# Kernel tuning notes

Measured on AMD Instinct MI355X. Metric: run time of the kernel, lower is better.

The kernel has to match this reference:

```python
import jax, jax.numpy as jnp
import numpy as np

B, Q, C, H, NSTEPS = 1024, 96, 16, 100, 100  # batch, q (MA order), channels, hidden, Euler steps


def setup_inputs() -> dict:
    key = jax.random.key(0)
    ks = jax.random.split(key, 6)
    s = 0.1  # weight init scale
    return {
        "series": jax.random.normal(ks[0], (B, Q, C), jnp.float32),
        "rand_error": jax.random.normal(ks[1], (B, 1, C), jnp.float32),
        "W1": jax.random.normal(ks[2], (H, Q + 2), jnp.float32) * s,
        "b1": jnp.zeros((H,), jnp.float32),
        "W2": jax.random.normal(ks[3], (H, H), jnp.float32) * s,
        "b2": jnp.zeros((H,), jnp.float32),
        "W3": jax.random.normal(ks[4], (Q + 1, H), jnp.float32) * s,
        "b3": jnp.zeros((Q + 1,), jnp.float32),
    }


def _mlp(x, t, W1, b1, W2, b2, W3, b3):
    # x: (B, Q+1, C), t: (B, 1, C)  -> cat along feature dim, permute to (B, C, Q+2)
    inp = jnp.concatenate([x, t], axis=1).transpose(0, 2, 1)
    h = jnp.tanh(inp @ W1.T + b1)
    h = jnp.tanh(h @ W2.T + b2)
    out = h @ W3.T + b3            # (B, C, Q+1)
    return out.transpose(0, 2, 1)  # (B, Q+1, C)


def reference(series, rand_error, W1, b1, W2, b2, W3, b3):
    # ma_forecast sampling path: noise = cat(series, rand_error) then Euler flow sampling
    noise = jnp.concatenate([series, rand_error], axis=1)  # (B, Q+1, C)
    dt = jnp.float32(1.0 / NSTEPS)

    def step(x, i):
        t = jnp.ones((x.shape[0], 1, x.shape[2]), x.dtype) * (i.astype(x.dtype) / NSTEPS)
        pred = _mlp(x, t, W1, b1, W2, b2, W3, b3)
        return x + (pred - noise) * dt, None

    x, _ = jax.lax.scan(step, noise, jnp.arange(NSTEPS))
    return x
```

## Files before the change

kernel.cpp:

```cpp
#include <hip/hip_runtime.h>


#define NB 1024
#define NQ 96
#define NC 16
#define NH 100
#define QP1 97
#define QP2 98
#define ROWS 16
#define NTHR 256
#define STR 136
#define NSTEPS_ 100

typedef __attribute__((ext_vector_type(8))) short bf16x8;
typedef __attribute__((ext_vector_type(4))) float f32x4;
typedef __attribute__((ext_vector_type(2))) unsigned uintx2;

__device__ __forceinline__ short f2bf_rne(float f) {
  unsigned u = __builtin_bit_cast(unsigned, f);
  u = u + 0x7fffu + ((u >> 16) & 1u);
  return (short)(u >> 16);
}

__device__ __forceinline__ unsigned bfhi(float f) {
  return (__builtin_bit_cast(unsigned, f) + 0x8000u) >> 16;
}

__device__ __forceinline__ unsigned pack_bf2(float a, float b) {
  unsigned ua = __builtin_bit_cast(unsigned, a) + 0x8000u;
  unsigned ub = __builtin_bit_cast(unsigned, b) + 0x8000u;
  return __builtin_amdgcn_perm(ub, ua, 0x07060302);
}

__device__ __forceinline__ float fast_tanh(float x) {
  float e = __builtin_amdgcn_exp2f(x * 2.88539008177792681f);
  float r = __builtin_amdgcn_rcpf(e + 1.0f);
  return fmaf(-2.0f, r, 1.0f);
}

__device__ void load_afrag(const float* __restrict__ W,
                           const float* __restrict__ bias, int ws, int mvalid,
                           int KW, int m, int quad, bf16x8 dst[4]) {
#pragma unroll
  for (int kb = 0; kb < 4; ++kb) {
    bf16x8 v;
#pragma unroll
    for (int i = 0; i < 8; ++i) {
      int k = kb * 32 + quad * 8 + i;
      float f = 0.0f;
      if (m < mvalid) {
        if (k < KW) f = W[m * ws + k];
        else if (k == KW) f = bias[m];
      }
      v[i] = f2bf_rne(f);
    }
    dst[kb] = v;
  }
}

__device__ __forceinline__ void gemm2(const short* __restrict__ src, int rbase,
                                      const bf16x8 (&A)[2][4], f32x4 (&acc)[2]) {
  acc[0] = {0.0f, 0.0f, 0.0f, 0.0f};
  acc[1] = {0.0f, 0.0f, 0.0f, 0.0f};
#pragma unroll
  for (int kb = 0; kb < 4; ++kb) {
    bf16x8 bv = *(const bf16x8*)(src + rbase + kb * 32);
    acc[0] = __builtin_amdgcn_mfma_f32_16x16x32_bf16(A[0][kb], bv, acc[0], 0, 0, 0);
    acc[1] = __builtin_amdgcn_mfma_f32_16x16x32_bf16(A[1][kb], bv, acc[1], 0, 0, 0);
  }
}

__device__ __forceinline__ void store_h(short* __restrict__ dst, int wb0,
                                        int wb1, bool fix100, f32x4 (&acc)[2]) {
#pragma unroll
  for (int mtl = 0; mtl < 2; ++mtl) {
    unsigned u0 = pack_bf2(fast_tanh(acc[mtl][0]), fast_tanh(acc[mtl][1]));
    unsigned u1 = pack_bf2(fast_tanh(acc[mtl][2]), fast_tanh(acc[mtl][3]));
    if (mtl == 0 && fix100) u0 = (u0 & 0xFFFF0000u) | 0x3F80u;
    uintx2 v;
    v.x = u0;
    v.y = u1;
    *(uintx2*)(dst + (mtl ? wb1 : wb0)) = v;
  }
}

__device__ __forceinline__ void write_x(short* __restrict__ dst, int wb0,
                                        int wb1, bool fix96, unsigned tbits,
                                        f32x4 (&xm)[2]) {
#pragma unroll
  for (int mtl = 0; mtl < 2; ++mtl) {
    unsigned u0 = pack_bf2(xm[mtl][0], xm[mtl][1]);
    unsigned u1 = pack_bf2(xm[mtl][2], xm[mtl][3]);
    if (mtl == 0 && fix96) {
      u0 = (u0 & 0x0000FFFFu) | (tbits << 16);
      u1 = 0x00003F80u;
    }
    uintx2 v;
    v.x = u0;
    v.y = u1;
    *(uintx2*)(dst + (mtl ? wb1 : wb0)) = v;
  }
}

__global__ void __launch_bounds__(NTHR, 3)
arima_mfma_t(const float* __restrict__ series,
             const float* __restrict__ rand_error,
             const float* __restrict__ W1, const float* __restrict__ b1,
             const float* __restrict__ W2, const float* __restrict__ b2,
             const float* __restrict__ W3, const float* __restrict__ b3,
             float* __restrict__ out) {
  __shared__ __align__(16) short bufP[ROWS * STR];
  __shared__ __align__(16) short bufQ[ROWS * STR];

  const int tid = threadIdx.x;
  const int w = tid >> 6, l = tid & 63;
  const int col = l & 15, quad = l >> 4;
  const int mt0 = 2 * w;
  const int bglob = (int)blockIdx.x;

  bf16x8 afr[3][2][4];
#pragma unroll
  for (int mtl = 0; mtl < 2; ++mtl) {
    int m = (mt0 + mtl) * 16 + col;
    load_afrag(W1, b1, QP2, NH, QP2, m, quad, afr[0][mtl]);
    load_afrag(W2, b2, NH, NH, NH, m, quad, afr[1][mtl]);
    load_afrag(W3, b3, NH, QP1, NH, m, quad, afr[2][mtl]);
  }

  f32x4 xm[2], ns[2];
#pragma unroll
  for (int mtl = 0; mtl < 2; ++mtl)
#pragma unroll
    for (int r = 0; r < 4; ++r) {
      int q = (mt0 + mtl) * 16 + quad * 4 + r;
      float f = 0.0f;
      if (q < NQ) f = series[(bglob * NQ + q) * NC + col];
      else if (q == NQ) f = rand_error[bglob * NC + col];
      xm[mtl][r] = f;
      ns[mtl][r] = f;
    }

  const int wb0 = col * STR + (mt0 + 0) * 16 + quad * 4;
  const int wb1 = col * STR + (mt0 + 1) * 16 + quad * 4;
  const int base0 = (mt0 + 0) * 16 + quad * 4;
  const bool fix100 = (base0 == 100);
  const bool fix96 = (base0 == 96);
  const int rbase = col * STR + quad * 8;

  write_x(bufP, wb0, wb1, fix96, 0u , xm);
  __syncthreads();

  short* bx = bufP;
  short* bh = bufQ;

#pragma unroll 1
  for (int step = 0; step < NSTEPS_; ++step) {
    f32x4 acc[2];
    gemm2(bx, rbase, afr[0], acc);
    store_h(bh, wb0, wb1, fix100, acc);
    __syncthreads();
    gemm2(bh, rbase, afr[1], acc);
    store_h(bx, wb0, wb1, fix100, acc);
    __syncthreads();
    gemm2(bx, rbase, afr[2], acc);
#pragma unroll
    for (int mtl = 0; mtl < 2; ++mtl)
#pragma unroll
      for (int r = 0; r < 4; ++r)
        xm[mtl][r] = fmaf(acc[mtl][r] - ns[mtl][r], 0.01f, xm[mtl][r]);
    float t1 = (float)(step + 1) / 100.0f;
    write_x(bh, wb0, wb1, fix96, bfhi(t1), xm);
    __syncthreads();

    short* tp = bx;
    bx = bh;
    bh = tp;
  }

#pragma unroll
  for (int mtl = 0; mtl < 2; ++mtl)
#pragma unroll
    for (int r = 0; r < 4; ++r) {
      int q = (mt0 + mtl) * 16 + quad * 4 + r;
      if (q < QP1) out[(bglob * QP1 + q) * NC + col] = xm[mtl][r];
    }
}

extern "C" void kernel_launch(void* const* d_in, const int* in_sizes, int n_in,
                              void* d_out, int out_size, void* d_ws,
                              size_t ws_size, hipStream_t stream) {
  const float* series = (const float*)d_in[0];
  const float* rand_error = (const float*)d_in[1];
  const float* W1 = (const float*)d_in[2];
  const float* b1 = (const float*)d_in[3];
  const float* W2 = (const float*)d_in[4];
  const float* b2 = (const float*)d_in[5];
  const float* W3 = (const float*)d_in[6];
  const float* b3 = (const float*)d_in[7];
  float* out = (float*)d_out;

  dim3 grid(NB);
  dim3 block(NTHR);
  hipLaunchKernelGGL(arima_mfma_t, grid, block, 0, stream, series, rand_error,
                     W1, b1, W2, b2, W3, b3, out);
}
```

Measured before the change: 290.1 us.

## Process two batch rows per block with split weight tiles and rational tanh

```diff
diff --git a/kernel.cpp b/kernel.cpp
--- a/kernel.cpp
+++ b/kernel.cpp
@@ -7,7 +7,7 @@
 #define NH 100
 #define QP1 97
 #define QP2 98
-#define ROWS 16
+#define ROWS 32
 #define NTHR 256
 #define STR 136
 #define NSTEPS_ 100
@@ -33,9 +33,11 @@
 }
 
 __device__ __forceinline__ float fast_tanh(float x) {
-  float e = __builtin_amdgcn_exp2f(x * 2.88539008177792681f);
-  float r = __builtin_amdgcn_rcpf(e + 1.0f);
-  return fmaf(-2.0f, r, 1.0f);
+  float u = x * x;
+  float num = x * fmaf(u + 105.0f, u, 945.0f);
+  float den = fmaf(fmaf(15.0f, u, 420.0f), u, 945.0f);
+  float v = num * __builtin_amdgcn_rcpf(den);
+  return fminf(fmaxf(v, -1.0f), 1.0f);
 }
 
 __device__ void load_afrag(const float* __restrict__ W,
@@ -58,132 +60,200 @@
   }
 }
 
-__device__ __forceinline__ void gemm2(const short* __restrict__ src, int rbase,
-                                      const bf16x8 (&A)[2][4], f32x4 (&acc)[2]) {
-  acc[0] = {0.0f, 0.0f, 0.0f, 0.0f};
-  acc[1] = {0.0f, 0.0f, 0.0f, 0.0f};
+template <int TC>
+__device__ __forceinline__ void gemmN(const short* __restrict__ src, int rbase,
+                                      const bf16x8 (&A)[TC][4],
+                                      f32x4 (&acc)[TC]) {
+#pragma unroll
+  for (int t = 0; t < TC; ++t) acc[t] = {0.0f, 0.0f, 0.0f, 0.0f};
 #pragma unroll
   for (int kb = 0; kb < 4; ++kb) {
     bf16x8 bv = *(const bf16x8*)(src + rbase + kb * 32);
-    acc[0] = __builtin_amdgcn_mfma_f32_16x16x32_bf16(A[0][kb], bv, acc[0], 0, 0, 0);
-    acc[1] = __builtin_amdgcn_mfma_f32_16x16x32_bf16(A[1][kb], bv, acc[1], 0, 0, 0);
-  }
-}
-
-__device__ __forceinline__ void store_h(short* __restrict__ dst, int wb0,
-                                        int wb1, bool fix100, f32x4 (&acc)[2]) {
-#pragma unroll
-  for (int mtl = 0; mtl < 2; ++mtl) {
-    unsigned u0 = pack_bf2(fast_tanh(acc[mtl][0]), fast_tanh(acc[mtl][1]));
-    unsigned u1 = pack_bf2(fast_tanh(acc[mtl][2]), fast_tanh(acc[mtl][3]));
-    if (mtl == 0 && fix100) u0 = (u0 & 0xFFFF0000u) | 0x3F80u;
-    uintx2 v;
-    v.x = u0;
-    v.y = u1;
-    *(uintx2*)(dst + (mtl ? wb1 : wb0)) = v;
-  }
-}
-
-__device__ __forceinline__ void write_x(short* __restrict__ dst, int wb0,
-                                        int wb1, bool fix96, unsigned tbits,
-                                        f32x4 (&xm)[2]) {
-#pragma unroll
-  for (int mtl = 0; mtl < 2; ++mtl) {
-    unsigned u0 = pack_bf2(xm[mtl][0], xm[mtl][1]);
-    unsigned u1 = pack_bf2(xm[mtl][2], xm[mtl][3]);
-    if (mtl == 0 && fix96) {
-      u0 = (u0 & 0x0000FFFFu) | (tbits << 16);
-      u1 = 0x00003F80u;
-    }
-    uintx2 v;
-    v.x = u0;
-    v.y = u1;
-    *(uintx2*)(dst + (mtl ? wb1 : wb0)) = v;
-  }
-}
-
-__global__ void __launch_bounds__(NTHR, 3)
-arima_mfma_t(const float* __restrict__ series,
-             const float* __restrict__ rand_error,
-             const float* __restrict__ W1, const float* __restrict__ b1,
-             const float* __restrict__ W2, const float* __restrict__ b2,
-             const float* __restrict__ W3, const float* __restrict__ b3,
-             float* __restrict__ out) {
+#pragma unroll
+    for (int t = 0; t < TC; ++t)
+      acc[t] = __builtin_amdgcn_mfma_f32_16x16x32_bf16(A[t][kb], bv, acc[t], 0, 0, 0);
+  }
+}
+
+template <int TC, int TO>
+__device__ __forceinline__ void store_h(short* __restrict__ dst, int wrow,
+                                        int quad, f32x4 (&acc)[TC]) {
+#pragma unroll
+  for (int t = 0; t < TC; ++t) {
+    unsigned u0 = pack_bf2(fast_tanh(acc[t][0]), fast_tanh(acc[t][1]));
+    unsigned u1 = pack_bf2(fast_tanh(acc[t][2]), fast_tanh(acc[t][3]));
+    if constexpr (TO + 0 <= 6 && 6 < TO + TC) {
+      if (TO + t == 6 && quad == 1) u0 = (u0 & 0xFFFF0000u) | 0x3F80u;
+    }
+    uintx2 v; v.x = u0; v.y = u1;
+    *(uintx2*)(dst + wrow + (TO + t) * 16 + quad * 4) = v;
+  }
+}
+
+template <int TC, int TO>
+__device__ __forceinline__ void write_x(short* __restrict__ dst, int wrow,
+                                        int quad, unsigned tbits,
+                                        f32x4 (&xm)[TC]) {
+#pragma unroll
+  for (int t = 0; t < TC; ++t) {
+    unsigned u0 = pack_bf2(xm[t][0], xm[t][1]);
+    unsigned u1 = pack_bf2(xm[t][2], xm[t][3]);
+    if constexpr (TO + 0 <= 6 && 6 < TO + TC) {
+      if (TO + t == 6 && quad == 0) {
+        u0 = (u0 & 0x0000FFFFu) | (tbits << 16);
+        u1 = 0x00003F80u;
+      }
+    }
+    uintx2 v; v.x = u0; v.y = u1;
+    *(uintx2*)(dst + wrow + (TO + t) * 16 + quad * 4) = v;
+  }
+}
+
+template <int TC1, int TO1, int TC2, int TO2, int TC3, int TO3>
+__device__ __forceinline__ void run_all(
+    const float* __restrict__ series, const float* __restrict__ rand_error,
+    const float* __restrict__ W1, const float* __restrict__ b1,
+    const float* __restrict__ W2, const float* __restrict__ b2,
+    const float* __restrict__ W3, const float* __restrict__ b3,
+    float* __restrict__ out, short* bufP, short* bufQ, int rw, int col,
+    int quad, int blk) {
+  bf16x8 a1[TC1][4], a2[TC2][4], a3[TC3][4];
+#pragma unroll
+  for (int t = 0; t < TC1; ++t)
+    load_afrag(W1, b1, QP2, NH, QP2, (TO1 + t) * 16 + col, quad, a1[t]);
+#pragma unroll
+  for (int t = 0; t < TC2; ++t)
+    load_afrag(W2, b2, NH, NH, NH, (TO2 + t) * 16 + col, quad, a2[t]);
+#pragma unroll
+  for (int t = 0; t < TC3; ++t)
+    load_afrag(W3, b3, NH, QP1, NH, (TO3 + t) * 16 + col, quad, a3[t]);
+
+  const int grow = blk * ROWS + rw * 16 + col;
+  const int gb = grow >> 4, gc = grow & 15;
+
+  f32x4 x0[TC3], xm[TC3];
+#pragma unroll
+  for (int t = 0; t < TC3; ++t)
+#pragma unroll
+    for (int r = 0; r < 4; ++r) {
+      int q = (TO3 + t) * 16 + quad * 4 + r;
+      float f = 0.0f;
+      if (q < NQ) f = series[(gb * NQ + q) * NC + gc];
+      else if (q == NQ) f = rand_error[gb * NC + gc];
+      x0[t][r] = f;
+      xm[t][r] = f;
+    }
+
+  const int wrow = (rw * 16 + col) * STR;
+  const int rbase = wrow + quad * 8;
+
+  write_x<TC3, TO3>(bufP, wrow, quad, 0u , xm);
+  __syncthreads();
+
+  short* bx = bufP;
+  short* bh = bufQ;
+
+#pragma unroll 1
+  for (int step = 0; step < NSTEPS_; ++step) {
+    {
+      f32x4 acc[TC1];
+      gemmN<TC1>(bx, rbase, a1, acc);
+      store_h<TC1, TO1>(bh, wrow, quad, acc);
+    }
+    __syncthreads();
+    {
+      f32x4 acc[TC2];
+      gemmN<TC2>(bh, rbase, a2, acc);
+      store_h<TC2, TO2>(bx, wrow, quad, acc);
+    }
+    __syncthreads();
+    {
+      f32x4 acc[TC3];
+      gemmN<TC3>(bx, rbase, a3, acc);
+#pragma unroll
+      for (int t = 0; t < TC3; ++t)
+#pragma unroll
+        for (int r = 0; r < 4; ++r)
+          xm[t][r] = fmaf(acc[t][r] - x0[t][r], 0.01f, xm[t][r]);
+      float t1 = (float)(step + 1) * 0.01f;
+      write_x<TC3, TO3>(bh, wrow, quad, bfhi(t1), xm);
+    }
+    __syncthreads();
+    short* tp = bx; bx = bh; bh = tp;
+  }
+
+#pragma unroll
+  for (int t = 0; t < TC3; ++t)
+#pragma unroll
+    for (int r = 0; r < 4; ++r) {
+      int q = (TO3 + t) * 16 + quad * 4 + r;
+      if (q < QP1) out[(gb * QP1 + q) * NC + gc] = xm[t][r];
+    }
+}
+
+__global__ void __launch_bounds__(NTHR, 2)
+arima_r4(const float* __restrict__ series, const float* __restrict__ rand_error,
+         const float* __restrict__ W1, const float* __restrict__ b1,
+         const float* __restrict__ W2, const float* __restrict__ b2,
+         const float* __restrict__ W3, const float* __restrict__ b3,
+         float* __restrict__ out) {
   __shared__ __align__(16) short bufP[ROWS * STR];
   __shared__ __align__(16) short bufQ[ROWS * STR];
 
   const int tid = threadIdx.x;
   const int w = tid >> 6, l = tid & 63;
   const int col = l & 15, quad = l >> 4;
-  const int mt0 = 2 * w;
-  const int bglob = (int)blockIdx.x;
-
-  bf16x8 afr[3][2][4];
-#pragma unroll
-  for (int mtl = 0; mtl < 2; ++mtl) {
-    int m = (mt0 + mtl) * 16 + col;
-    load_afrag(W1, b1, QP2, NH, QP2, m, quad, afr[0][mtl]);
-    load_afrag(W2, b2, NH, NH, NH, m, quad, afr[1][mtl]);
-    load_afrag(W3, b3, NH, QP1, NH, m, quad, afr[2][mtl]);
-  }
-
-  f32x4 xm[2], ns[2];
-#pragma unroll
-  for (int mtl = 0; mtl < 2; ++mtl)
-#pragma unroll
-    for (int r = 0; r < 4; ++r) {
-      int q = (mt0 + mtl) * 16 + quad * 4 + r;
-      float f = 0.0f;
-      if (q < NQ) f = series[(bglob * NQ + q) * NC + col];
-      else if (q == NQ) f = rand_error[bglob * NC + col];
-      xm[mtl][r] = f;
-      ns[mtl][r] = f;
-    }
-
-  const int wb0 = col * STR + (mt0 + 0) * 16 + quad * 4;
-  const int wb1 = col * STR + (mt0 + 1) * 16 + quad * 4;
-  const int base0 = (mt0 + 0) * 16 + quad * 4;
-  const bool fix100 = (base0 == 100);
-  const bool fix96 = (base0 == 96);
-  const int rbase = col * STR + quad * 8;
-
-  write_x(bufP, wb0, wb1, fix96, 0u , xm);
+  const int rw = w >> 1, nw = w & 1;
+
+  {
+    int* zp = (int*)bufP;
+    int* zq = (int*)bufQ;
+    for (int i = tid; i < ROWS * STR / 2; i += NTHR) { zp[i] = 0; zq[i] = 0; }
+  }
   __syncthreads();
 
-  short* bx = bufP;
-  short* bh = bufQ;
-
-#pragma unroll 1
-  for (int step = 0; step < NSTEPS_; ++step) {
-    f32x4 acc[2];
-    gemm2(bx, rbase, afr[0], acc);
-    store_h(bh, wb0, wb1, fix100, acc);
-    __syncthreads();
-    gemm2(bh, rbase, afr[1], acc);
-    store_h(bx, wb0, wb1, fix100, acc);
-    __syncthreads();
-    gemm2(bx, rbase, afr[2], acc);
-#pragma unroll
-    for (int mtl = 0; mtl < 2; ++mtl)
-#pragma unroll
-      for (int r = 0; r < 4; ++r)
-        xm[mtl][r] = fmaf(acc[mtl][r] - ns[mtl][r], 0.01f, xm[mtl][r]);
-    float t1 = (float)(step + 1) / 100.0f;
-    write_x(bh, wb0, wb1, fix96, bfhi(t1), xm);
-    __syncthreads();
-
-    short* tp = bx;
-    bx = bh;
-    bh = tp;
-  }
-
-#pragma unroll
-  for (int mtl = 0; mtl < 2; ++mtl)
-#pragma unroll
-    for (int r = 0; r < 4; ++r) {
-      int q = (mt0 + mtl) * 16 + quad * 4 + r;
-      if (q < QP1) out[(bglob * QP1 + q) * NC + col] = xm[mtl][r];
-    }
+  if (nw == 0) {
+    run_all<4, 0, 3, 0, 4, 0>(series, rand_error, W1, b1, W2, b2, W3, b3,
+                              (float*)nullptr ? nullptr : nullptr, bufP, bufQ,
+                              rw, col, quad, (int)blockIdx.x),
+        (void)0;
+  }
+  if (nw == 0) {
+  }
+  if (nw == 0) {
+  }
+}
+
+
+__global__ void __launch_bounds__(NTHR, 2)
+arima_r4_real(const float* __restrict__ series,
+              const float* __restrict__ rand_error,
+              const float* __restrict__ W1, const float* __restrict__ b1,
+              const float* __restrict__ W2, const float* __restrict__ b2,
+              const float* __restrict__ W3, const float* __restrict__ b3,
+              float* __restrict__ out) {
+  __shared__ __align__(16) short bufP[ROWS * STR];
+  __shared__ __align__(16) short bufQ[ROWS * STR];
+
+  const int tid = threadIdx.x;
+  const int w = tid >> 6, l = tid & 63;
+  const int col = l & 15, quad = l >> 4;
+  const int rw = w >> 1, nw = w & 1;
+
+  {
+    int* zp = (int*)bufP;
+    int* zq = (int*)bufQ;
+    for (int i = tid; i < ROWS * STR / 2; i += NTHR) { zp[i] = 0; zq[i] = 0; }
+  }
+  __syncthreads();
+
+  if (nw == 0) {
+    run_all<4, 0, 3, 0, 4, 0>(series, rand_error, W1, b1, W2, b2, W3, b3, out,
+                              bufP, bufQ, rw, col, quad, (int)blockIdx.x);
+  } else {
+    run_all<3, 4, 4, 3, 3, 4>(series, rand_error, W1, b1, W2, b2, W3, b3, out,
+                              bufP, bufQ, rw, col, quad, (int)blockIdx.x);
+  }
 }
 
 extern "C" void kernel_launch(void* const* d_in, const int* in_sizes, int n_in,
@@ -199,8 +269,8 @@
   const float* b3 = (const float*)d_in[7];
   float* out = (float*)d_out;
 
-  dim3 grid(NB);
+  dim3 grid((NB * NC) / ROWS);
   dim3 block(NTHR);
-  hipLaunchKernelGGL(arima_mfma_t, grid, block, 0, stream, series, rand_error,
+  hipLaunchKernelGGL(arima_r4_real, grid, block, 0, stream, series, rand_error,
                      W1, b1, W2, b2, W3, b3, out);
 }
```

Result: slower. 321.3 us (+10.7%).

## Fold W1·W3 into a precomputed matrix and update layer-1 pre-activations directly

Applied to the files above, without the earlier changes.

```diff
diff --git a/kernel.cpp b/kernel.cpp
--- a/kernel.cpp
+++ b/kernel.cpp
@@ -7,10 +7,10 @@
 #define NH 100
 #define QP1 97
 #define QP2 98
-#define ROWS 16
 #define NTHR 256
 #define STR 136
 #define NSTEPS_ 100
+#define MT_K 128
 
 typedef __attribute__((ext_vector_type(8))) short bf16x8;
 typedef __attribute__((ext_vector_type(4))) float f32x4;
@@ -22,10 +22,6 @@
   return (short)(u >> 16);
 }
 
-__device__ __forceinline__ unsigned bfhi(float f) {
-  return (__builtin_bit_cast(unsigned, f) + 0x8000u) >> 16;
-}
-
 __device__ __forceinline__ unsigned pack_bf2(float a, float b) {
   unsigned ua = __builtin_bit_cast(unsigned, a) + 0x8000u;
   unsigned ub = __builtin_bit_cast(unsigned, b) + 0x8000u;
@@ -33,9 +29,36 @@
 }
 
 __device__ __forceinline__ float fast_tanh(float x) {
-  float e = __builtin_amdgcn_exp2f(x * 2.88539008177792681f);
-  float r = __builtin_amdgcn_rcpf(e + 1.0f);
-  return fmaf(-2.0f, r, 1.0f);
+  float u = x * x;
+  float num = x * fmaf(u + 105.0f, u, 945.0f);
+  float den = fmaf(fmaf(15.0f, u, 420.0f), u, 945.0f);
+  float v = num * __builtin_amdgcn_rcpf(den);
+  return fminf(fmaxf(v, -1.0f), 1.0f);
+}
+
+__global__ void __launch_bounds__(128) arima_prep(
+    const float* __restrict__ W1, const float* __restrict__ b1,
+    const float* __restrict__ W3, const float* __restrict__ b3,
+    short* __restrict__ Mt, float* __restrict__ sv) {
+  const int n = blockIdx.x;
+  const int k = threadIdx.x;
+  float acc = 0.0f;
+  if (n < NH && k < NH) {
+#pragma unroll 1
+    for (int j = 0; j < QP1; ++j)
+      acc = fmaf(W1[n * QP2 + j], W3[j * NH + k], acc);
+  }
+  Mt[n * MT_K + k] = f2bf_rne(0.01f * acc);
+  if (k == 0) {
+    float s = 0.0f;
+    if (n < NH) {
+      float d = 0.0f;
+#pragma unroll 1
+      for (int j = 0; j < QP1; ++j) d = fmaf(W1[n * QP2 + j], b3[j], d);
+      s = 0.01f * (d + b1[n] + W1[n * QP2 + QP1]);
+    }
+    sv[n] = s;
+  }
 }
 
 __device__ void load_afrag(const float* __restrict__ W,
@@ -58,10 +81,9 @@
   }
 }
 
-__device__ __forceinline__ void gemm2(const short* __restrict__ src, int rbase,
-                                      const bf16x8 (&A)[2][4], f32x4 (&acc)[2]) {
-  acc[0] = {0.0f, 0.0f, 0.0f, 0.0f};
-  acc[1] = {0.0f, 0.0f, 0.0f, 0.0f};
+__device__ __forceinline__ void gemm_acc(const short* __restrict__ src,
+                                         int rbase, const bf16x8 (&A)[2][4],
+                                         f32x4 (&acc)[2]) {
 #pragma unroll
   for (int kb = 0; kb < 4; ++kb) {
     bf16x8 bv = *(const bf16x8*)(src + rbase + kb * 32);
@@ -70,120 +92,146 @@
   }
 }
 
-__device__ __forceinline__ void store_h(short* __restrict__ dst, int wb0,
-                                        int wb1, bool fix100, f32x4 (&acc)[2]) {
-#pragma unroll
-  for (int mtl = 0; mtl < 2; ++mtl) {
-    unsigned u0 = pack_bf2(fast_tanh(acc[mtl][0]), fast_tanh(acc[mtl][1]));
-    unsigned u1 = pack_bf2(fast_tanh(acc[mtl][2]), fast_tanh(acc[mtl][3]));
-    if (mtl == 0 && fix100) u0 = (u0 & 0xFFFF0000u) | 0x3F80u;
-    uintx2 v;
-    v.x = u0;
-    v.y = u1;
-    *(uintx2*)(dst + (mtl ? wb1 : wb0)) = v;
-  }
-}
-
-__device__ __forceinline__ void write_x(short* __restrict__ dst, int wb0,
-                                        int wb1, bool fix96, unsigned tbits,
-                                        f32x4 (&xm)[2]) {
-#pragma unroll
-  for (int mtl = 0; mtl < 2; ++mtl) {
-    unsigned u0 = pack_bf2(xm[mtl][0], xm[mtl][1]);
-    unsigned u1 = pack_bf2(xm[mtl][2], xm[mtl][3]);
-    if (mtl == 0 && fix96) {
-      u0 = (u0 & 0x0000FFFFu) | (tbits << 16);
-      u1 = 0x00003F80u;
-    }
-    uintx2 v;
-    v.x = u0;
-    v.y = u1;
-    *(uintx2*)(dst + (mtl ? wb1 : wb0)) = v;
-  }
+__device__ __forceinline__ void write_tiles(short* __restrict__ dst, int wrow,
+                                            int T0, int quad, const f32x4& v0,
+                                            const f32x4& v1) {
+  uintx2 a, b;
+  a.x = pack_bf2(v0[0], v0[1]);
+  a.y = pack_bf2(v0[2], v0[3]);
+  b.x = pack_bf2(v1[0], v1[1]);
+  b.y = pack_bf2(v1[2], v1[3]);
+  *(uintx2*)(dst + wrow + T0 * 16 + quad * 4) = a;
+  *(uintx2*)(dst + wrow + (T0 + 1) * 16 + quad * 4) = b;
 }
 
 __global__ void __launch_bounds__(NTHR, 3)
-arima_mfma_t(const float* __restrict__ series,
-             const float* __restrict__ rand_error,
-             const float* __restrict__ W1, const float* __restrict__ b1,
-             const float* __restrict__ W2, const float* __restrict__ b2,
-             const float* __restrict__ W3, const float* __restrict__ b3,
-             float* __restrict__ out) {
-  __shared__ __align__(16) short bufP[ROWS * STR];
-  __shared__ __align__(16) short bufQ[ROWS * STR];
+arima_r5(const float* __restrict__ series, const float* __restrict__ rand_error,
+         const float* __restrict__ W1, const float* __restrict__ b1,
+         const float* __restrict__ W2, const float* __restrict__ b2,
+         const float* __restrict__ W3, const float* __restrict__ b3,
+         const short* __restrict__ Mt, const float* __restrict__ sv,
+         float* __restrict__ out) {
+  __shared__ __align__(16) short buf1[16 * STR];
+  __shared__ __align__(16) short buf2[16 * STR];
 
   const int tid = threadIdx.x;
   const int w = tid >> 6, l = tid & 63;
   const int col = l & 15, quad = l >> 4;
-  const int mt0 = 2 * w;
-  const int bglob = (int)blockIdx.x;
-
-  bf16x8 afr[3][2][4];
-#pragma unroll
-  for (int mtl = 0; mtl < 2; ++mtl) {
-    int m = (mt0 + mtl) * 16 + col;
-    load_afrag(W1, b1, QP2, NH, QP2, m, quad, afr[0][mtl]);
-    load_afrag(W2, b2, NH, NH, NH, m, quad, afr[1][mtl]);
-    load_afrag(W3, b3, NH, QP1, NH, m, quad, afr[2][mtl]);
-  }
-
-  f32x4 xm[2], ns[2];
-#pragma unroll
-  for (int mtl = 0; mtl < 2; ++mtl)
-#pragma unroll
-    for (int r = 0; r < 4; ++r) {
-      int q = (mt0 + mtl) * 16 + quad * 4 + r;
-      float f = 0.0f;
-      if (q < NQ) f = series[(bglob * NQ + q) * NC + col];
-      else if (q == NQ) f = rand_error[bglob * NC + col];
-      xm[mtl][r] = f;
-      ns[mtl][r] = f;
-    }
-
-  const int wb0 = col * STR + (mt0 + 0) * 16 + quad * 4;
-  const int wb1 = col * STR + (mt0 + 1) * 16 + quad * 4;
-  const int base0 = (mt0 + 0) * 16 + quad * 4;
-  const bool fix100 = (base0 == 100);
-  const bool fix96 = (base0 == 96);
-  const int rbase = col * STR + quad * 8;
-
-  write_x(bufP, wb0, wb1, fix96, 0u , xm);
+  const int b = blockIdx.x;
+  const int T0 = 2 * w;
+  const int wrow = col * STR;
+  const int rbase = wrow + quad * 8;
+  const bool fixw = (w == 3 && quad == 1);
+
+  {
+    f32x4 xv[2];
+#pragma unroll
+    for (int t = 0; t < 2; ++t)
+#pragma unroll
+      for (int r = 0; r < 4; ++r) {
+        int q = (T0 + t) * 16 + quad * 4 + r;
+        float f = 0.0f;
+        if (q < NQ) f = series[(b * NQ + q) * NC + col];
+        else if (q == NQ) f = rand_error[b * NC + col];
+        else if (q == QP2) f = 1.0f;
+        xv[t][r] = f;
+      }
+    write_tiles(buf2, wrow, T0, quad, xv[0], xv[1]);
+  }
   __syncthreads();
 
-  short* bx = bufP;
-  short* bh = bufQ;
+  f32x4 z[2], v[2];
+  {
+    bf16x8 a1[2][4];
+#pragma unroll
+    for (int t = 0; t < 2; ++t)
+      load_afrag(W1, b1, QP2, NH, QP2, (T0 + t) * 16 + col, quad, a1[t]);
+    z[0] = {0.0f, 0.0f, 0.0f, 0.0f};
+    z[1] = {0.0f, 0.0f, 0.0f, 0.0f};
+    gemm_acc(buf2, rbase, a1, z);
+#pragma unroll
+    for (int t = 0; t < 2; ++t)
+#pragma unroll
+      for (int r = 0; r < 4; ++r)
+        v[t][r] = sv[(T0 + t) * 16 + quad * 4 + r] - 0.01f * z[t][r];
+  }
+  {
+    f32x4 h[2];
+#pragma unroll
+    for (int t = 0; t < 2; ++t)
+#pragma unroll
+      for (int r = 0; r < 4; ++r) h[t][r] = fast_tanh(z[t][r]);
+    if (fixw) h[0][0] = 1.0f;
+    write_tiles(buf1, wrow, T0, quad, h[0], h[1]);
+  }
+  __syncthreads();
+
+  bf16x8 a2[2][4], am[2][4];
+#pragma unroll
+  for (int t = 0; t < 2; ++t) {
+    load_afrag(W2, b2, NH, NH, NH, (T0 + t) * 16 + col, quad, a2[t]);
+#pragma unroll
+    for (int kb = 0; kb < 4; ++kb)
+      am[t][kb] = *(const bf16x8*)(Mt + ((T0 + t) * 16 + col) * MT_K +
+                                   kb * 32 + quad * 8);
+  }
+  f32x4 h2s[2] = {{0.0f, 0.0f, 0.0f, 0.0f}, {0.0f, 0.0f, 0.0f, 0.0f}};
 
 #pragma unroll 1
   for (int step = 0; step < NSTEPS_; ++step) {
-    f32x4 acc[2];
-    gemm2(bx, rbase, afr[0], acc);
-    store_h(bh, wb0, wb1, fix100, acc);
+    f32x4 acc[2], h[2];
+    acc[0] = {0.0f, 0.0f, 0.0f, 0.0f};
+    acc[1] = {0.0f, 0.0f, 0.0f, 0.0f};
+    gemm_acc(buf1, rbase, a2, acc);
+#pragma unroll
+    for (int t = 0; t < 2; ++t)
+#pragma unroll
+      for (int r = 0; r < 4; ++r) {
+        h[t][r] = fast_tanh(acc[t][r]);
+        h2s[t][r] += h[t][r];
+      }
+    write_tiles(buf2, wrow, T0, quad, h[0], h[1]);
     __syncthreads();
-    gemm2(bh, rbase, afr[1], acc);
-    store_h(bx, wb0, wb1, fix100, acc);
+    gemm_acc(buf2, rbase, am, z);
+#pragma unroll
+    for (int t = 0; t < 2; ++t)
+#pragma unroll
+      for (int r = 0; r < 4; ++r) {
+        z[t][r] += v[t][r];
+        h[t][r] = fast_tanh(z[t][r]);
+      }
+    if (fixw) h[0][0] = 1.0f;
+    write_tiles(buf1, wrow, T0, quad, h[0], h[1]);
     __syncthreads();
-    gemm2(bx, rbase, afr[2], acc);
-#pragma unroll
-    for (int mtl = 0; mtl < 2; ++mtl)
-#pragma unroll
-      for (int r = 0; r < 4; ++r)
-        xm[mtl][r] = fmaf(acc[mtl][r] - ns[mtl][r], 0.01f, xm[mtl][r]);
-    float t1 = (float)(step + 1) / 100.0f;
-    write_x(bh, wb0, wb1, fix96, bfhi(t1), xm);
-    __syncthreads();
-
-    short* tp = bx;
-    bx = bh;
-    bh = tp;
-  }
-
-#pragma unroll
-  for (int mtl = 0; mtl < 2; ++mtl)
-#pragma unroll
-    for (int r = 0; r < 4; ++r) {
-      int q = (mt0 + mtl) * 16 + quad * 4 + r;
-      if (q < QP1) out[(bglob * QP1 + q) * NC + col] = xm[mtl][r];
-    }
+  }
+
+  {
+    f32x4 ha[2];
+#pragma unroll
+    for (int t = 0; t < 2; ++t)
+#pragma unroll
+      for (int r = 0; r < 4; ++r) ha[t][r] = 0.01f * h2s[t][r];
+    if (fixw) ha[0][0] = 1.0f;
+    write_tiles(buf2, wrow, T0, quad, ha[0], ha[1]);
+  }
+  __syncthreads();
+  {
+    bf16x8 a3[2][4];
+#pragma unroll
+    for (int t = 0; t < 2; ++t)
+      load_afrag(W3, b3, NH, QP1, NH, (T0 + t) * 16 + col, quad, a3[t]);
+    f32x4 o[2];
+    o[0] = {0.0f, 0.0f, 0.0f, 0.0f};
+    o[1] = {0.0f, 0.0f, 0.0f, 0.0f};
+    gemm_acc(buf2, rbase, a3, o);
+#pragma unroll
+    for (int t = 0; t < 2; ++t)
+#pragma unroll
+      for (int r = 0; r < 4; ++r) {
+        int q = (T0 + t) * 16 + quad * 4 + r;
+        if (q < QP1) out[(b * QP1 + q) * NC + col] = o[t][r];
+      }
+  }
 }
 
 extern "C" void kernel_launch(void* const* d_in, const int* in_sizes, int n_in,
@@ -199,8 +247,11 @@
   const float* b3 = (const float*)d_in[7];
   float* out = (float*)d_out;
 
-  dim3 grid(NB);
-  dim3 block(NTHR);
-  hipLaunchKernelGGL(arima_mfma_t, grid, block, 0, stream, series, rand_error,
-                     W1, b1, W2, b2, W3, b3, out);
-}
+  short* Mt = (short*)d_ws;
+  float* sv = (float*)((char*)d_ws + 128 * 128 * 2);
+
+  hipLaunchKernelGGL(arima_prep, dim3(128), dim3(128), 0, stream, W1, b1, W3,
+                     b3, Mt, sv);
+  hipLaunchKernelGGL(arima_r5, dim3(NB), dim3(NTHR), 0, stream, series,
+                     rand_error, W1, b1, W2, b2, W3, b3, Mt, sv, out);
+}
```

After: 289.0 us. About the same (-0.4%).
